# Optimization experiments

Hardware: AMD Instinct MI355X
Metric: run time of the kernel (lower is better)

## Reference

```python
import jax, jax.numpy as jnp
import numpy as np

N_HIDDEN = 96
N_LAYER = 4
IN_FEAT = 24


def _lstm_layer(xs, W_ih, W_hh, b):
    # xs: [T, B, in]; W_ih: [4H, in]; W_hh: [4H, H]; b: [4H]
    B = xs.shape[1]
    h0 = jnp.zeros((B, N_HIDDEN), xs.dtype)
    c0 = jnp.zeros((B, N_HIDDEN), xs.dtype)

    def step(carry, x_t):
        h, c = carry
        gates = x_t @ W_ih.T + h @ W_hh.T + b  # [B, 4H], torch gate order i,f,g,o
        i, f, g, o = jnp.split(gates, 4, axis=-1)
        i = jax.nn.sigmoid(i)
        f = jax.nn.sigmoid(f)
        g = jnp.tanh(g)
        o = jax.nn.sigmoid(o)
        c = f * c + i * g
        h = o * jnp.tanh(c)
        return (h, c), h

    (hT, cT), ys = jax.lax.scan(step, (h0, c0), xs)
    return ys, hT


def setup_inputs() -> dict:
    key = jax.random.key(0)
    ks = jax.random.split(key, 16)
    B, T = 4096, 128
    k = 1.0 / np.sqrt(N_HIDDEN)  # torch default LSTM init bound
    u = lambda kk, shape: jax.random.uniform(kk, shape, jnp.float32, -k, k)
    inp = {
        "x": jax.random.normal(ks[0], (B, T, IN_FEAT), jnp.float32),
        "W_ih0": u(ks[1], (4 * N_HIDDEN, IN_FEAT)),          # layer 0 input weights
        "W_ih_rest": u(ks[2], (N_LAYER - 1, 4 * N_HIDDEN, N_HIDDEN)),  # layers 1..3
        "W_hh": u(ks[3], (N_LAYER, 4 * N_HIDDEN, N_HIDDEN)),
        "b_ih": u(ks[4], (N_LAYER, 4 * N_HIDDEN)),
        "b_hh": u(ks[5], (N_LAYER, 4 * N_HIDDEN)),
        "fc1_w": u(ks[6], (16, N_HIDDEN)),
        "fc1_b": u(ks[7], (16,)),
        "fc2_w": u(ks[8], (8, 16)),
        "fc2_b": u(ks[9], (8,)),
        "fc3_w": u(ks[10], (1, 8)),
        "fc3_b": u(ks[11], (1,)),
    }
    return inp


def reference(x, W_ih0, W_ih_rest, W_hh, b_ih, b_hh,
              fc1_w, fc1_b, fc2_w, fc2_b, fc3_w, fc3_b):
    # x: [B, T, F] (batch_first); scan over time -> [T, B, F]
    xs = jnp.transpose(x, (1, 0, 2))
    hns = []
    ys, h = _lstm_layer(xs, W_ih0, W_hh[0], b_ih[0] + b_hh[0])
    hns.append(h)
    for l in range(N_LAYER - 1):  # inter-layer dropout p=0.1 -> identity in eval
        ys, h = _lstm_layer(ys, W_ih_rest[l], W_hh[l + 1], b_ih[l + 1] + b_hh[l + 1])
        hns.append(h)
    # original forward detaches hn via numpy round-trip -> stop_gradient
    hn_sum = jax.lax.stop_gradient(hns[-1] + hns[1])  # [B, H]
    z = jax.nn.relu(hn_sum)
    z = jax.nn.relu(z @ fc1_w.T + fc1_b)
    z = jax.nn.relu(z @ fc2_w.T + fc2_b)
    out = z @ fc3_w.T + fc3_b  # head dropout p=0.1 -> identity in eval
    return out  # [B, 1]
```

## Files before the change

### kernel.cpp

```cpp
#include <hip/hip_runtime.h>
#include <math.h>

typedef _Float16 f16;
typedef _Float16 f16x8 __attribute__((ext_vector_type(8)));
typedef float f32x4 __attribute__((ext_vector_type(4)));
typedef float f32x2 __attribute__((ext_vector_type(2)));

#define B_TOTAL 4096
#define T_STEPS 128
#define H 96
#define NB 16
#define NTH 768
#define NBLK (B_TOTAL/NB)
#define GUP 97
#define ST_T (NB*H)
#define LOG2E 1.44269504088896f

__device__ __forceinline__ float sig2(float vp){
    return __builtin_amdgcn_rcpf(1.f + __builtin_amdgcn_exp2f(-vp));
}
__device__ __forceinline__ float tanh2(float vpp){
    return 1.f - 2.f*__builtin_amdgcn_rcpf(__builtin_amdgcn_exp2f(vpp) + 1.f);
}
__device__ __forceinline__ float tanh_c(float c){
    return tanh2(c * (2.f*LOG2E));
}

__device__ __forceinline__ void lds_barrier(){
    __builtin_amdgcn_sched_barrier(0);
    asm volatile("s_waitcnt lgkmcnt(0)" ::: "memory");
    __builtin_amdgcn_s_barrier();
    __builtin_amdgcn_sched_barrier(0);
}

template<int F, bool IS_L0, bool HAS_YSOUT, bool WRITE_HSUM, bool ADD_HSUM>
__device__ __forceinline__ void layer_run(
    const float* __restrict__ x32, f16* __restrict__ strip,
    const float* __restrict__ Wi, const float* __restrict__ Wh,
    const float* __restrict__ bi, const float* __restrict__ bh,
    f16* sh, f16* sl, float* gbuf, float* hsum, int row0)
{
    constexpr int  KS   = (F + H + 31)/32;
    constexpr int  KP   = KS*32;
    constexpr int  KPB  = KP*2;
    constexpr bool HAS_LO = IS_L0;
    constexpr int  BUF  = 16*KP;

    const int tid=threadIdx.x, lane=tid&63, w=tid>>6;
    const int j15=lane&15, g4=lane>>4;
    const int g=w>>1, q0=(w&1)*2;
    const int u=16*g+j15;
    const int eu=tid>>3, er0=(tid&7)*2;
    const int sr=tid/48, su=(tid-sr*48)*2;
    const int ysrd_off = sr*KPB + (((F+su)*2) ^ ((sr&7)<<4));

    for (int i=tid;i<2*BUF;i+=NTH) sh[i]=(f16)0.f;
    if constexpr (HAS_LO)
        for (int i=tid;i<2*BUF;i+=NTH) sl[i]=(f16)0.f;

    f16x8 Bf[2][KS];
    float scl[2];
#pragma unroll
    for (int qq=0;qq<2;++qq) scl[qq] = (q0+qq==2) ? 2.f*LOG2E : LOG2E;
#pragma unroll
    for (int qq=0;qq<2;++qq){
        const int j=96*(q0+qq)+u;
#pragma unroll
        for (int s=0;s<KS;++s){
            f16x8 f;
#pragma unroll
            for (int e=0;e<8;++e){
                int k=32*s+8*g4+e;
                float v=0.f;
                if (k<F)        v=Wi[(size_t)j*F+k];
                else if (k-F<H) v=Wh[(size_t)j*H+(k-F)];
                f[e]=(f16)(v*scl[qq]);
            }
            Bf[qq][s]=f;
        }
    }
    float bq[2];
#pragma unroll
    for (int qq=0;qq<2;++qq)
        bq[qq]=(bi[96*(q0+qq)+u]+bh[96*(q0+qq)+u])*scl[qq];

    float c2[2]={0.f,0.f};

    unsigned*       ysst = (unsigned*)strip + tid;
    const unsigned* yld  = (const unsigned*)strip + (ST_T/2) + tid;
    const int yr=(tid*2)/H, yk=(tid*2)-yr*H;
    const int yoff = yr*KPB + ((yk*2)^((yr&7)<<4));

    const int xr=tid/24, xk=tid-xr*24;
    const bool xact = IS_L0 && (tid < NB*24);
    const float* xbase = xact ? x32 + (size_t)(row0+xr)*(T_STEPS*24) + xk : nullptr;
    const int xoff = xr*KPB + ((xk*2)^((xr&7)<<4));

    if constexpr (IS_L0){
        if (xact){
            float v=xbase[0];
            f16 vh=(f16)v, vl=(f16)(v-(float)vh);
            *(f16*)((char*)sh+xoff)=vh; *(f16*)((char*)sl+xoff)=vl;
        }
    } else {
        unsigned v = *((const unsigned*)strip + tid);
        *(unsigned*)((char*)sh+yoff)=v;
    }
    __syncthreads();

    unsigned yvA=0u;
    if constexpr (!IS_L0){ yvA = *yld; yld += ST_T/2; }

    const int aswz=(j15&7)<<4;
    const int abase=j15*KPB;
    int gw[4];
#pragma unroll
    for (int r=0;r<4;++r) gw[r]=(((4*g4+r)*GUP+u)*4+q0)*4;
    int grd[2], nho[2];
#pragma unroll
    for (int s2=0;s2<2;++s2){
        grd[s2]=((er0+s2)*GUP+eu)*16;
        nho[s2]=(er0+s2)*KPB + (((F+eu)*2)^(((er0+s2)&7)<<4));
    }

#pragma unroll 1
    for (int t=0;t<T_STEPS;++t){
        const int cur=t&1, nxt=cur^1;
        const char* chb=(const char*)(sh+cur*BUF);
        const char* clb=HAS_LO ? (const char*)(sl+cur*BUF) : nullptr;
        char*       nhb=(char*)(sh+nxt*BUF);
        char*       nlb=HAS_LO ? (char*)(sl+nxt*BUF) : nullptr;

        float xv=0.f; unsigned yvB=0u;
        if constexpr (IS_L0){
            if (xact && t+1<T_STEPS) xv = xbase[(size_t)(t+1)*24];
        } else {
            if (t+2<T_STEPS){ yvB = *yld; yld += ST_T/2; }
        }
        __builtin_amdgcn_sched_barrier(0);

        unsigned hbits=0u;
        if (HAS_YSOUT && t>0) hbits = *(const unsigned*)(chb + ysrd_off);

        f32x4 acc[2][2];
#pragma unroll
        for (int qq=0;qq<2;++qq){
            f32x4 a={bq[qq],bq[qq],bq[qq],bq[qq]}; acc[qq][0]=a;
            f32x4 z={0.f,0.f,0.f,0.f};              acc[qq][1]=z;
        }
#pragma unroll
        for (int s=0;s<KS;++s){
            int kb=((s*64+g4*16)^aswz);
            f16x8 ah=*(const f16x8*)(chb+abase+kb);
            if (s&1){
                acc[0][1]=__builtin_amdgcn_mfma_f32_16x16x32_f16(ah,Bf[0][s],acc[0][1],0,0,0);
                acc[1][1]=__builtin_amdgcn_mfma_f32_16x16x32_f16(ah,Bf[1][s],acc[1][1],0,0,0);
            } else {
                acc[0][0]=__builtin_amdgcn_mfma_f32_16x16x32_f16(ah,Bf[0][s],acc[0][0],0,0,0);
                acc[1][0]=__builtin_amdgcn_mfma_f32_16x16x32_f16(ah,Bf[1][s],acc[1][0],0,0,0);
            }
        }
        if constexpr (HAS_LO){
            int kb=((g4*16)^aswz);
            f16x8 al=*(const f16x8*)(clb+abase+kb);
            acc[0][1]=__builtin_amdgcn_mfma_f32_16x16x32_f16(al,Bf[0][0],acc[0][1],0,0,0);
            acc[1][1]=__builtin_amdgcn_mfma_f32_16x16x32_f16(al,Bf[1][0],acc[1][1],0,0,0);
        }
#pragma unroll
        for (int r=0;r<4;++r){
            float v0=acc[0][0][r]+acc[0][1][r];
            float v1=acc[1][0][r]+acc[1][1][r];
            float a0 = (q0==0) ? sig2(v0) : tanh2(v0);
            float a1 = sig2(v1);
            f32x2 p={a0,a1};
            *(f32x2*)((char*)gbuf + gw[r]) = p;
        }
        lds_barrier();

        if (HAS_YSOUT && t>0){ *ysst = hbits; ysst += ST_T/2; }

#pragma unroll
        for (int s2=0;s2<2;++s2){
            f32x4 gv4 = *(const f32x4*)((const char*)gbuf + grd[s2]);
            float c = gv4[1]*c2[s2] + gv4[0]*gv4[2];
            c2[s2]=c;
            float h = gv4[3]*tanh_c(c);
            *(f16*)(nhb + nho[s2]) = (f16)h;
            if constexpr (WRITE_HSUM){ if (t==T_STEPS-1) hsum[(er0+s2)*96+eu]=h; }
            if constexpr (ADD_HSUM)  { if (t==T_STEPS-1) hsum[(er0+s2)*96+eu]+=h; }
        }
        if (t+1<T_STEPS){
            if constexpr (IS_L0){
                if (xact){
                    f16 vh=(f16)xv, vl=(f16)(xv-(float)vh);
                    *(f16*)(nhb+xoff)=vh; *(f16*)(nlb+xoff)=vl;
                }
            } else {
                *(unsigned*)(nhb+yoff)=yvA;
            }
        }
        lds_barrier();
        yvA = yvB;
    }
    if constexpr (HAS_YSOUT){
        unsigned hbits = *(const unsigned*)((const char*)sh + ysrd_off);
        asm volatile("s_waitcnt lgkmcnt(0)" ::: "memory");
        *ysst = hbits;
    }
}

__global__ __launch_bounds__(NTH, 1)
void lstm_all(const float* __restrict__ x,
              const float* __restrict__ W_ih0,
              const float* __restrict__ W_ih_rest,
              const float* __restrict__ W_hh,
              const float* __restrict__ b_ih,
              const float* __restrict__ b_hh,
              const float* __restrict__ fc1_w, const float* __restrict__ fc1_b,
              const float* __restrict__ fc2_w, const float* __restrict__ fc2_b,
              const float* __restrict__ fc3_w, const float* __restrict__ fc3_b,
              f16* __restrict__ ws_strip, float* __restrict__ out)
{
    __shared__ f16 sh[2*16*192];
    __shared__ f16 sl[2*16*128];
    __shared__ float gbuf[16*GUP*4];
    __shared__ float hsum[16*96];
    __shared__ float z1[16*16];
    __shared__ float z2[16*8];

    const int tid=threadIdx.x;
    const int b=blockIdx.x, row0=b*NB;
    f16* strip = ws_strip + (size_t)b*T_STEPS*ST_T;
    const int GH = 384*96;

    layer_run<24, true,  true,  false, false>(x, strip, W_ih0,             W_hh,        b_ih,          b_hh,          sh,sl,gbuf,hsum,row0);
    __syncthreads();
    layer_run<96, false, true,  true,  false>(nullptr, strip, W_ih_rest,        W_hh+1*GH, b_ih+1*384, b_hh+1*384, sh,sl,gbuf,hsum,row0);
    __syncthreads();
    layer_run<96, false, true,  false, false>(nullptr, strip, W_ih_rest+1*GH, W_hh+2*GH, b_ih+2*384, b_hh+2*384, sh,sl,gbuf,hsum,row0);
    __syncthreads();
    layer_run<96, false, false, false, true >(nullptr, strip, W_ih_rest+2*GH, W_hh+3*GH, b_ih+3*384, b_hh+3*384, sh,sl,gbuf,hsum,row0);
    __syncthreads();

    if (tid<256){
        int r=tid>>4, jj=tid&15;
        float a=fc1_b[jj];
        for (int uu=0;uu<96;++uu) a+=fc1_w[jj*96+uu]*fmaxf(hsum[r*96+uu],0.f);
        z1[r*16+jj]=fmaxf(a,0.f);
    }
    __syncthreads();
    if (tid<128){
        int r=tid>>3, jj=tid&7;
        float a=fc2_b[jj];
#pragma unroll
        for (int uu=0;uu<16;++uu) a+=fc2_w[jj*16+uu]*z1[r*16+uu];
        z2[r*8+jj]=fmaxf(a,0.f);
    }
    __syncthreads();
    if (tid<16){
        float a=fc3_b[0];
#pragma unroll
        for (int uu=0;uu<8;++uu) a+=fc3_w[uu]*z2[tid*8+uu];
        out[row0+tid]=a;
    }
}

extern "C" void kernel_launch(void* const* d_in, const int* in_sizes, int n_in,
                              void* d_out, int out_size, void* d_ws, size_t ws_size,
                              hipStream_t stream) {
    const float* x         = (const float*)d_in[0];
    const float* W_ih0     = (const float*)d_in[1];
    const float* W_ih_rest = (const float*)d_in[2];
    const float* W_hh      = (const float*)d_in[3];
    const float* b_ih      = (const float*)d_in[4];
    const float* b_hh      = (const float*)d_in[5];
    const float* fc1_w     = (const float*)d_in[6];
    const float* fc1_b     = (const float*)d_in[7];
    const float* fc2_w     = (const float*)d_in[8];
    const float* fc2_b     = (const float*)d_in[9];
    const float* fc3_w     = (const float*)d_in[10];
    const float* fc3_b     = (const float*)d_in[11];
    float* out = (float*)d_out;

    const size_t WS = (size_t)NBLK * T_STEPS * ST_T * sizeof(f16);
    if (ws_size < WS) {
        hipMemsetAsync(d_out, 0, (size_t)out_size * sizeof(float), stream);
        return;
    }

    lstm_all<<<dim3(NBLK), dim3(NTH), 0, stream>>>(
        x, W_ih0, W_ih_rest, W_hh, b_ih, b_hh,
        fc1_w, fc1_b, fc2_w, fc2_b, fc3_w, fc3_b,
        (f16*)d_ws, out);
}
```

Before: 581.8 us.

## Reassign gate pairs per wave to shrink LDS gate exchange

```diff
diff --git a/kernel.cpp b/kernel.cpp
--- a/kernel.cpp
+++ b/kernel.cpp
@@ -12,7 +12,6 @@
 #define NB 16
 #define NTH 768
 #define NBLK (B_TOTAL/NB)
-#define GUP 97
 #define ST_T (NB*H)
 #define LOG2E 1.44269504088896f
 
@@ -38,7 +37,7 @@
     const float* __restrict__ x32, f16* __restrict__ strip,
     const float* __restrict__ Wi, const float* __restrict__ Wh,
     const float* __restrict__ bi, const float* __restrict__ bh,
-    f16* sh, f16* sl, float* gbuf, float* hsum, int row0)
+    f16* sh, f16* sl, float* p_lds, float* hsum, int row0)
 {
     constexpr int  KS   = (F + H + 31)/32;
     constexpr int  KP   = KS*32;
@@ -48,9 +47,9 @@
 
     const int tid=threadIdx.x, lane=tid&63, w=tid>>6;
     const int j15=lane&15, g4=lane>>4;
-    const int g=w>>1, q0=(w&1)*2;
+    const int g=w>>1;
+    const int qsel=w&1;
     const int u=16*g+j15;
-    const int eu=tid>>3, er0=(tid&7)*2;
     const int sr=tid/48, su=(tid-sr*48)*2;
     const int ysrd_off = sr*KPB + (((F+su)*2) ^ ((sr&7)<<4));
 
@@ -61,10 +60,13 @@
     f16x8 Bf[2][KS];
     float scl[2];
 #pragma unroll
-    for (int qq=0;qq<2;++qq) scl[qq] = (q0+qq==2) ? 2.f*LOG2E : LOG2E;
-#pragma unroll
     for (int qq=0;qq<2;++qq){
-        const int j=96*(q0+qq)+u;
+        int qg = qsel + 2*qq;
+        scl[qq] = (qg==2) ? 2.f*LOG2E : LOG2E;
+    }
+#pragma unroll
+    for (int qq=0;qq<2;++qq){
+        const int j=96*(qsel+2*qq)+u;
 #pragma unroll
         for (int s=0;s<KS;++s){
             f16x8 f;
@@ -82,9 +84,9 @@
     float bq[2];
 #pragma unroll
     for (int qq=0;qq<2;++qq)
-        bq[qq]=(bi[96*(q0+qq)+u]+bh[96*(q0+qq)+u])*scl[qq];
-
-    float c2[2]={0.f,0.f};
+        bq[qq]=(bi[96*(qsel+2*qq)+u]+bh[96*(qsel+2*qq)+u])*scl[qq];
+
+    float c4[4]={0.f,0.f,0.f,0.f};
 
     unsigned*       ysst = (unsigned*)strip + tid;
     const unsigned* yld  = (const unsigned*)strip + (ST_T/2) + tid;
@@ -113,14 +115,13 @@
 
     const int aswz=(j15&7)<<4;
     const int abase=j15*KPB;
-    int gw[4];
-#pragma unroll
-    for (int r=0;r<4;++r) gw[r]=(((4*g4+r)*GUP+u)*4+q0)*4;
-    int grd[2], nho[2];
-#pragma unroll
-    for (int s2=0;s2<2;++s2){
-        grd[s2]=((er0+s2)*GUP+eu)*16;
-        nho[s2]=(er0+s2)*KPB + (((F+eu)*2)^(((er0+s2)&7)<<4));
+    const int pbase = (g*64+lane)*16;
+    int nhoB[4], hsiB[4];
+#pragma unroll
+    for (int r=0;r<4;++r){
+        int row=4*g4+r;
+        nhoB[r]=row*KPB + (((F+u)*2)^((row&7)<<4));
+        hsiB[r]=row*96+u;
     }
 
 #pragma unroll 1
@@ -166,28 +167,42 @@
             acc[0][1]=__builtin_amdgcn_mfma_f32_16x16x32_f16(al,Bf[0][0],acc[0][1],0,0,0);
             acc[1][1]=__builtin_amdgcn_mfma_f32_16x16x32_f16(al,Bf[1][0],acc[1][1],0,0,0);
         }
-#pragma unroll
-        for (int r=0;r<4;++r){
-            float v0=acc[0][0][r]+acc[0][1][r];
-            float v1=acc[1][0][r]+acc[1][1][r];
-            float a0 = (q0==0) ? sig2(v0) : tanh2(v0);
-            float a1 = sig2(v1);
-            f32x2 p={a0,a1};
-            *(f32x2*)((char*)gbuf + gw[r]) = p;
+
+        float af[4], ao[4];
+        if (qsel==0){
+#pragma unroll
+            for (int pr=0;pr<2;++pr){
+                float i0=sig2(acc[0][0][2*pr  ]+acc[0][1][2*pr  ]);
+                float i1=sig2(acc[0][0][2*pr+1]+acc[0][1][2*pr+1]);
+                float g0=tanh2(acc[1][0][2*pr  ]+acc[1][1][2*pr  ]);
+                float g1=tanh2(acc[1][0][2*pr+1]+acc[1][1][2*pr+1]);
+                f32x2 p={i0*g0, i1*g1};
+                *(f32x2*)((char*)p_lds + pbase + pr*8) = p;
+            }
+        } else {
+#pragma unroll
+            for (int r=0;r<4;++r){
+                af[r]=sig2(acc[0][0][r]+acc[0][1][r]);
+                ao[r]=sig2(acc[1][0][r]+acc[1][1][r]);
+            }
         }
         lds_barrier();
 
         if (HAS_YSOUT && t>0){ *ysst = hbits; ysst += ST_T/2; }
 
-#pragma unroll
-        for (int s2=0;s2<2;++s2){
-            f32x4 gv4 = *(const f32x4*)((const char*)gbuf + grd[s2]);
-            float c = gv4[1]*c2[s2] + gv4[0]*gv4[2];
-            c2[s2]=c;
-            float h = gv4[3]*tanh_c(c);
-            *(f16*)(nhb + nho[s2]) = (f16)h;
-            if constexpr (WRITE_HSUM){ if (t==T_STEPS-1) hsum[(er0+s2)*96+eu]=h; }
-            if constexpr (ADD_HSUM)  { if (t==T_STEPS-1) hsum[(er0+s2)*96+eu]+=h; }
+        if (qsel==1){
+            f32x2 pA = *(const f32x2*)((const char*)p_lds + pbase);
+            f32x2 pB = *(const f32x2*)((const char*)p_lds + pbase + 8);
+            float p4[4]={pA[0],pA[1],pB[0],pB[1]};
+#pragma unroll
+            for (int r=0;r<4;++r){
+                float c = af[r]*c4[r] + p4[r];
+                c4[r]=c;
+                float h = ao[r]*tanh_c(c);
+                *(f16*)(nhb + nhoB[r]) = (f16)h;
+                if constexpr (WRITE_HSUM){ if (t==T_STEPS-1) hsum[hsiB[r]]=h; }
+                if constexpr (ADD_HSUM)  { if (t==T_STEPS-1) hsum[hsiB[r]]+=h; }
+            }
         }
         if (t+1<T_STEPS){
             if constexpr (IS_L0){
@@ -223,7 +238,7 @@
 {
     __shared__ f16 sh[2*16*192];
     __shared__ f16 sl[2*16*128];
-    __shared__ float gbuf[16*GUP*4];
+    __shared__ float p_lds[6*64*4];
     __shared__ float hsum[16*96];
     __shared__ float z1[16*16];
     __shared__ float z2[16*8];
@@ -233,13 +248,13 @@
     f16* strip = ws_strip + (size_t)b*T_STEPS*ST_T;
     const int GH = 384*96;
 
-    layer_run<24, true,  true,  false, false>(x, strip, W_ih0,             W_hh,        b_ih,          b_hh,          sh,sl,gbuf,hsum,row0);
-    __syncthreads();
-    layer_run<96, false, true,  true,  false>(nullptr, strip, W_ih_rest,        W_hh+1*GH, b_ih+1*384, b_hh+1*384, sh,sl,gbuf,hsum,row0);
-    __syncthreads();
-    layer_run<96, false, true,  false, false>(nullptr, strip, W_ih_rest+1*GH, W_hh+2*GH, b_ih+2*384, b_hh+2*384, sh,sl,gbuf,hsum,row0);
-    __syncthreads();
-    layer_run<96, false, false, false, true >(nullptr, strip, W_ih_rest+2*GH, W_hh+3*GH, b_ih+3*384, b_hh+3*384, sh,sl,gbuf,hsum,row0);
+    layer_run<24, true,  true,  false, false>(x, strip, W_ih0,             W_hh,        b_ih,          b_hh,          sh,sl,p_lds,hsum,row0);
+    __syncthreads();
+    layer_run<96, false, true,  true,  false>(nullptr, strip, W_ih_rest,        W_hh+1*GH, b_ih+1*384, b_hh+1*384, sh,sl,p_lds,hsum,row0);
+    __syncthreads();
+    layer_run<96, false, true,  false, false>(nullptr, strip, W_ih_rest+1*GH, W_hh+2*GH, b_ih+2*384, b_hh+2*384, sh,sl,p_lds,hsum,row0);
+    __syncthreads();
+    layer_run<96, false, false, false, true >(nullptr, strip, W_ih_rest+2*GH, W_hh+3*GH, b_ih+3*384, b_hh+3*384, sh,sl,p_lds,hsum,row0);
     __syncthreads();
 
     if (tid<256){
```

New measurement: 561.5 us. -3.5%, faster.
